# Performance work log

Measured on AMD Instinct MI355X. Metric: run time of the kernel, lower is better.

## Reference

```python
import jax, jax.numpy as jnp
import numpy as np
import math

NUM_CONVS = 4
GN_GROUPS = 32
GN_EPS = 1e-5
FPN_STRIDES = (8, 16, 32, 64, 128)
PRIOR_PROB = 0.01


def conv3x3(x, w, b):
    # x: [N,C,H,W], w: [O,I,3,3]
    y = jax.lax.conv_general_dilated(
        x, w, window_strides=(1, 1), padding='SAME',
        dimension_numbers=('NCHW', 'OIHW', 'NCHW'))
    return y + b[None, :, None, None]


def group_norm(x, gamma, beta):
    n, c, h, w = x.shape
    xg = x.reshape(n, GN_GROUPS, c // GN_GROUPS, h, w)
    mean = xg.mean(axis=(2, 3, 4), keepdims=True)
    var = xg.var(axis=(2, 3, 4), keepdims=True)
    xn = ((xg - mean) * jax.lax.rsqrt(var + GN_EPS)).reshape(n, c, h, w)
    return xn * gamma[None, :, None, None] + beta[None, :, None, None]


def subnet(x, ws, bs, gws, gbs):
    # NUM_CONVS x (conv3x3 -> GN -> ReLU)
    for i in range(NUM_CONVS):
        x = jax.nn.relu(group_norm(conv3x3(x, ws[i], bs[i]), gws[i], gbs[i]))
    return x


def permute_to_N_HWA_K(x, k):
    n = x.shape[0]
    return x.transpose(0, 2, 3, 1).reshape(n, -1, k)


def setup_inputs() -> dict:
    key = jax.random.key(0)
    ks = jax.random.split(key, 16)
    C, K = 256, 80
    feats = {
        'p3': jax.random.normal(ks[0], (1, C, 80, 80), jnp.float32),
        'p4': jax.random.normal(ks[1], (1, C, 40, 40), jnp.float32),
        'p5': jax.random.normal(ks[2], (1, C, 20, 20), jnp.float32),
        'p6': jax.random.normal(ks[3], (1, C, 10, 10), jnp.float32),
        'p7': jax.random.normal(ks[4], (1, C, 5, 5), jnp.float32),
    }
    std = 0.01
    bias_value = -math.log((1 - PRIOR_PROB) / PRIOR_PROB)
    params = {
        'cls_w': std * jax.random.normal(ks[5], (NUM_CONVS, C, C, 3, 3), jnp.float32),
        'cls_b': jnp.zeros((NUM_CONVS, C), jnp.float32),
        'cls_gn_w': jnp.ones((NUM_CONVS, C), jnp.float32),
        'cls_gn_b': jnp.zeros((NUM_CONVS, C), jnp.float32),
        'box_w': std * jax.random.normal(ks[6], (NUM_CONVS, C, C, 3, 3), jnp.float32),
        'box_b': jnp.zeros((NUM_CONVS, C), jnp.float32),
        'box_gn_w': jnp.ones((NUM_CONVS, C), jnp.float32),
        'box_gn_b': jnp.zeros((NUM_CONVS, C), jnp.float32),
        'score_w': std * jax.random.normal(ks[7], (K, C, 3, 3), jnp.float32),
        'score_b': jnp.full((K,), bias_value, jnp.float32),
        'pred_w': std * jax.random.normal(ks[8], (4, C, 3, 3), jnp.float32),
        'pred_b': jnp.zeros((4,), jnp.float32),
        'iou_w': std * jax.random.normal(ks[9], (1, C, 3, 3), jnp.float32),
        'iou_b': jnp.zeros((1,), jnp.float32),
        'scales': jnp.ones((5,), jnp.float32),
    }
    return {**feats, **params}


def reference(p3, p4, p5, p6, p7,
              cls_w, cls_b, cls_gn_w, cls_gn_b,
              box_w, box_b, box_gn_w, box_gn_b,
              score_w, score_b, pred_w, pred_b, iou_w, iou_b, scales):
    features = [p3, p4, p5, p6, p7]
    logits, bbox_reg, ious = [], [], []
    for l, feat in enumerate(features):
        c = subnet(feat, cls_w, cls_b, cls_gn_w, cls_gn_b)
        b = subnet(feat, box_w, box_b, box_gn_w, box_gn_b)
        logit = conv3x3(c, score_w, score_b)          # [N,80,H,W]
        iou = conv3x3(b, iou_w, iou_b)                # [N,1,H,W]
        bp = conv3x3(b, pred_w, pred_b) * scales[l]   # Scale module
        # norm_reg_targets=True branch
        reg = jax.nn.relu(bp) * FPN_STRIDES[l]        # [N,4,H,W]
        logits.append(permute_to_N_HWA_K(logit, 80))
        bbox_reg.append(permute_to_N_HWA_K(reg, 4))
        ious.append(permute_to_N_HWA_K(iou, 1))
    box_cls = jnp.concatenate(logits, axis=1)    # [N, sumHW, 80]
    box_delta = jnp.concatenate(bbox_reg, axis=1)  # [N, sumHW, 4]
    box_iou = jnp.concatenate(ious, axis=1)      # [N, sumHW, 1]
    # pack into one array for a single output: [N, sumHW, 85]
    return jnp.concatenate([box_cls, box_delta, box_iou], axis=-1)
```

## Files before the change

### kernel.cpp

```cpp
#include <hip/hip_runtime.h>

typedef unsigned short u16;
typedef __attribute__((ext_vector_type(8))) short bf16x8;
typedef __attribute__((ext_vector_type(4))) float f32x4;

#define NLEV 5
#define CCH 256
#define KTOT 2304
#define P_TOT 8525
#define PP_TOT 9165
#define PLS (PP_TOT*64)

__constant__ int   c_HW[NLEV]     = {6400, 1600, 400, 100, 25};
__constant__ int   c_W[NLEV]      = {80, 40, 20, 10, 5};
__constant__ int   c_off[NLEV]    = {0, 6400, 8000, 8400, 8500};
__constant__ int   c_poff[NLEV]   = {0, 6724, 8488, 8972, 9116};
__constant__ int   c_tls[NLEV+1]  = {0, 50, 65, 71, 73, 74};
__constant__ int   c_ntx[NLEV]    = {5, 3, 2, 1, 1};
__constant__ float c_stridef[NLEV]= {8.f, 16.f, 32.f, 64.f, 128.f};

__device__ __forceinline__ u16 f2bf(float f){
  union { float f; unsigned u; } v; v.f = f;
  unsigned r = v.u + 0x7fffu + ((v.u >> 16) & 1u);
  return (u16)(r >> 16);
}

__device__ __forceinline__ void g2l16(const u16* g, u16* l, int lane){
#if defined(__has_builtin)
#if __has_builtin(__builtin_amdgcn_global_load_lds)
  __builtin_amdgcn_global_load_lds(
      (const __attribute__((address_space(1))) unsigned int*)g,
      (__attribute__((address_space(3))) unsigned int*)l, 16, 0, 0);
  return;
#endif
#endif
  *(uint4*)(l + lane*8) = *(const uint4*)g;
}

#define WAIT_VM0_LGKM0 0x0070

template<int MODE>
__global__ __launch_bounds__(256, 2) void gemm_conv(
    const u16* __restrict__ Xc, const u16* __restrict__ Xb,
    const u16* __restrict__ Wc, const u16* __restrict__ Wb,
    const float* __restrict__ bc, const float* __restrict__ bb,
    float* __restrict__ Yc, float* __restrict__ Yb,
    float* __restrict__ stats,
    const float* __restrict__ predb, const float* __restrict__ ioub,
    const float* __restrict__ scales, float* __restrict__ out)
{
  __shared__ u16 sA0[8192], sA1[8192];
  __shared__ u16 hB0[23*512], hB1[23*512];
  __shared__ float sstat[16][2];

  const int ptile = blockIdx.x;
  const int mtile = (MODE == 0) ? blockIdx.y : 0;
  const int br = blockIdx.z;
  int lv = 0;
  #pragma unroll
  for (int i = 1; i < NLEV; i++) if (ptile >= c_tls[i]) lv = i;
  const int tidx = ptile - c_tls[lv];
  const int ntx = c_ntx[lv];
  const int ty0 = (tidx / ntx) * 8, tx0 = (tidx - (tidx / ntx) * ntx) * 16;
  const int W = c_W[lv], wrow2 = W + 2;

  const int tid = threadIdx.x, wv = tid >> 6, ln = tid & 63;
  const int quad = ln >> 4, l15 = ln & 15;
  const int m0w = (wv & 1) * 64;
  const int pyw = (wv >> 1) * 4;

  const u16* __restrict__ X  = br ? Xb : Xc;
  const u16* __restrict__ WA = br ? Wb : Wc;

  const int ASTRIDE = (MODE == 0) ? 16384 : 8192;
  const u16* abase = WA + (size_t)(((MODE == 0) ? mtile*16 : 0) + wv*4)*512 + ln*8;

  const u16* hptr[6]; int hnum = 0;
  #pragma unroll
  for (int i = 0; i < 6; i++) {
    const int j = wv + 4*i;
    if (j < 23) {
      const int item = j*64 + ln;
      int hp = item >> 3; if (hp >= 180) hp -= 180;
      const int g = item & 7;
      const int hy = hp / 18, hx = hp - hy*18;
      const int prow = c_poff[lv] + (ty0 + hy)*wrow2 + tx0 + hx;
      hptr[i] = X + (size_t)prow*64 + ((g ^ (hp & 7)) << 3);
      hnum = i + 1;
    }
  }

  auto stageA = [&](int cc, int tap, u16* dA) {
    const u16* as = abase + (size_t)(tap*4 + cc) * ASTRIDE;
    u16* da = dA + (wv*4)*512;
    #pragma unroll
    for (int j = 0; j < 4; j++) g2l16(as + j*512, da + j*512, ln);
  };
  auto stageH = [&](int cc, u16* dH) {
    const size_t cof = (size_t)cc * PLS;
    for (int i = 0; i < hnum; i++)
      g2l16(hptr[i] + cof, dH + (wv + 4*i)*512, ln);
  };

  f32x4 acc[4][4];
  #pragma unroll
  for (int i = 0; i < 4; i++)
    #pragma unroll
    for (int j = 0; j < 4; j++) acc[i][j] = (f32x4){0.f, 0.f, 0.f, 0.f};

  if (MODE == 0 && tid < 32) sstat[tid >> 1][tid & 1] = 0.f;

  auto kbody = [&](int t, const u16* rA, u16* wA2) {
    __builtin_amdgcn_sched_barrier(0);
    __builtin_amdgcn_s_waitcnt(WAIT_VM0_LGKM0);
    __builtin_amdgcn_sched_barrier(0);
    __builtin_amdgcn_s_barrier();
    __builtin_amdgcn_sched_barrier(0);
    const int cc = t / 9, tap = t - cc*9;
    if (t < 35) {
      const int t1 = t + 1, ncc = t1 / 9;
      stageA(ncc, t1 - ncc*9, wA2);
    }
    if (tap == 8 && cc < 3) stageH(cc + 1, ((cc + 1) & 1) ? hB1 : hB0);
    const u16* rB = (cc & 1) ? hB1 : hB0;
    const int dh = tap / 3, dw = tap - dh*3;
    bf16x8 af[2][4], bf[2][4];
    #pragma unroll
    for (int sub = 0; sub < 2; sub++) {
      const int swzA = ((sub*4 + quad) ^ (l15 & 7)) * 8;
      #pragma unroll
      for (int mt = 0; mt < 4; mt++)
        af[sub][mt] = *(const bf16x8*)&rA[(m0w + mt*16 + l15)*64 + swzA];
      #pragma unroll
      for (int nt = 0; nt < 4; nt++) {
        const int hp = (pyw + nt + dh)*18 + l15 + dw;
        const int gk = sub*4 + quad;
        bf[sub][nt] = *(const bf16x8*)&rB[hp*64 + ((gk ^ (hp & 7)) << 3)];
      }
    }
    #pragma unroll
    for (int sub = 0; sub < 2; sub++)
      #pragma unroll
      for (int mt = 0; mt < 4; mt++)
        #pragma unroll
        for (int nt = 0; nt < 4; nt++)
          acc[mt][nt] = __builtin_amdgcn_mfma_f32_16x16x32_bf16(
              af[sub][mt], bf[sub][nt], acc[mt][nt], 0, 0, 0);
  };

  stageH(0, hB0);
  stageA(0, 0, sA0);
  #pragma unroll 1
  for (int t = 0; t < 36; t += 2) {
    kbody(t,     sA0, sA1);
    kbody(t + 1, sA1, sA0);
  }

  const int gx = tx0 + l15;
  if (MODE == 0) {
    const float* __restrict__ bias = br ? bb : bc;
    float* __restrict__ Y = br ? Yb : Yc;
    #pragma unroll
    for (int mt = 0; mt < 4; mt++) {
      const int mloc = m0w + mt*16 + quad*4;
      const int mrow = mtile*128 + mloc;
      const f32x4 bv = *(const f32x4*)&bias[mrow];
      float s = 0.f, sq = 0.f;
      #pragma unroll
      for (int nt = 0; nt < 4; nt++) {
        const int gy = ty0 + pyw + nt;
        f32x4 v = acc[mt][nt] + bv;
        if (gy < W && gx < W) {
          const size_t n = (size_t)(c_off[lv] + gy*W + gx);
          *(f32x4*)&Y[n*CCH + mrow] = v;
          #pragma unroll
          for (int r = 0; r < 4; r++) { s += v[r]; sq += v[r]*v[r]; }
        }
      }
      #pragma unroll
      for (int o = 1; o < 16; o <<= 1) { s += __shfl_xor(s, o); sq += __shfl_xor(sq, o); }
      if (l15 == 0) {
        const int g = mloc >> 3;
        atomicAdd(&sstat[g][0], s);
        atomicAdd(&sstat[g][1], sq);
      }
    }
    __syncthreads();
    if (tid < 32) {
      const int g = tid >> 1, c = tid & 1;
      atomicAdd(&stats[((br*NLEV + lv)*32 + mtile*16 + g)*2 + c], sstat[g][c]);
    }
  } else {
    const float scl = scales[lv];
    const float stf = c_stridef[lv];
    #pragma unroll
    for (int mt = 0; mt < 4; mt++) {
      const int mr0 = m0w + mt*16 + quad*4;
      if (mr0 >= 85) continue;
      #pragma unroll
      for (int nt = 0; nt < 4; nt++) {
        const int gy = ty0 + pyw + nt;
        if (gy >= W || gx >= W) continue;
        const size_t n = (size_t)(c_off[lv] + gy*W + gx);
        const f32x4 v = acc[mt][nt];
        #pragma unroll
        for (int r = 0; r < 4; r++) {
          const int m = mr0 + r;
          if (br == 0) {
            if (m < 80) out[n*85 + m] = v[r] + bc[m];
          } else {
            if (m < 4) {
              const float t = (v[r] + predb[m]) * scl;
              out[n*85 + 80 + m] = fmaxf(t, 0.f) * stf;
            } else if (m == 4) {
              out[n*85 + 84] = v[r] + ioub[0];
            }
          }
        }
      }
    }
  }
}

__global__ __launch_bounds__(256) void gn_relu(
    const float* __restrict__ Yc, const float* __restrict__ Yb,
    const float* __restrict__ stats,
    const float* __restrict__ gwc, const float* __restrict__ gbc,
    const float* __restrict__ gwb, const float* __restrict__ gbb,
    u16* __restrict__ Xc, u16* __restrict__ Xb)
{
  const int t = blockIdx.x * 256 + threadIdx.x;
  if (t >= 2 * P_TOT * 32) return;
  const int br = t / (P_TOT * 32);
  const int r  = t - br * (P_TOT * 32);
  const int pg = r >> 5;
  const int c0 = (r & 31) << 3;
  int lv = 0;
  #pragma unroll
  for (int i = 1; i < NLEV; i++) if (pg >= c_off[i]) lv = i;
  const int pl = pg - c_off[lv];
  const int Wl = c_W[lv];
  const int g = c0 >> 3;
  const float* st = &stats[(((size_t)br*NLEV + lv)*32 + g)*2];
  const float cnt = 8.f * (float)c_HW[lv];
  const float mean = st[0] / cnt;
  const float var  = st[1] / cnt - mean*mean;
  const float rstd = rsqrtf(var + 1e-5f);
  const float* Y  = br ? Yb : Yc;
  const float* gw = br ? gwb : gwc;
  const float* gb = br ? gbb : gbc;
  u16* X = br ? Xb : Xc;
  const float* y = &Y[(size_t)pg*CCH + c0];
  const int h = pl / Wl, wi = pl - h*Wl;
  const size_t pidx = (size_t)(c_poff[lv] + (h+1)*(Wl+2) + (wi+1));
  union { u16 u[8]; uint4 v; } pk;
  #pragma unroll
  for (int i = 0; i < 8; i++) {
    const float v = (y[i] - mean)*rstd*gw[c0+i] + gb[c0+i];
    pk.u[i] = f2bf(fmaxf(v, 0.f));
  }
  *(uint4*)&X[(size_t)(c0 >> 6)*PLS + pidx*64 + (c0 & 63)] = pk.v;
}

__global__ __launch_bounds__(256) void feat2bf(
    const float* __restrict__ p3, const float* __restrict__ p4,
    const float* __restrict__ p5, const float* __restrict__ p6,
    const float* __restrict__ p7, u16* __restrict__ X)
{
  const int t = blockIdx.x * 256 + threadIdx.x;
  if (t >= P_TOT * 32) return;
  const int pg = t >> 5, c0 = (t & 31) << 3;
  int lv = 0;
  #pragma unroll
  for (int i = 1; i < NLEV; i++) if (pg >= c_off[i]) lv = i;
  const int pl = pg - c_off[lv];
  const float* src = lv==0 ? p3 : lv==1 ? p4 : lv==2 ? p5 : lv==3 ? p6 : p7;
  const int HW = c_HW[lv], Wl = c_W[lv];
  const int h = pl / Wl, wi = pl - h*Wl;
  const size_t pidx = (size_t)(c_poff[lv] + (h+1)*(Wl+2) + (wi+1));
  union { u16 u[8]; uint4 v; } pk;
  #pragma unroll
  for (int i = 0; i < 8; i++)
    pk.u[i] = f2bf(src[(size_t)(c0+i)*HW + pl]);
  *(uint4*)&X[(size_t)(c0 >> 6)*PLS + pidx*64 + (c0 & 63)] = pk.v;
}

__global__ __launch_bounds__(256) void wconv(
    const float* __restrict__ cw, const float* __restrict__ bw,
    u16* __restrict__ Wc, u16* __restrict__ Wb)
{
  const size_t N = (size_t)4*256*KTOT;
  const size_t t = (size_t)blockIdx.x * 256 + threadIdx.x;
  if (t >= 2*N) return;
  const float* src = (t < N) ? cw : bw;
  u16* dst = (t < N) ? Wc : Wb;
  const size_t i = (t < N) ? t : t - N;
  const size_t lc = i / KTOT;
  const int kk = (int)(i - lc*KTOT);
  const int l = (int)(lc >> 8), co = (int)(lc & 255);
  const int tap = kk >> 8, ci = kk & 255;
  const int s = kk >> 6, kl = kk & 63;
  const int r = co & 7, p = (kl >> 3) ^ r;
  const size_t d = (size_t)l*589824 +
      ((size_t)((s*32 + (co >> 3))*64 + r*8 + p))*8 + (kl & 7);
  dst[d] = f2bf(src[(lc*256 + ci)*9 + tap]);
}

__global__ __launch_bounds__(256) void hconv(
    const float* __restrict__ sw, const float* __restrict__ pw,
    const float* __restrict__ iw, u16* __restrict__ Whc, u16* __restrict__ Whb)
{
  const int N = 128 * KTOT;
  const int t = blockIdx.x * 256 + threadIdx.x;
  if (t >= 2*N) return;
  const int i = (t < N) ? t : t - N;
  const int co = i / KTOT, kk = i - co*KTOT;
  const int tap = kk >> 8, ci = kk & 255;
  const int s = kk >> 6, kl = kk & 63;
  const int r = co & 7, p = (kl >> 3) ^ r;
  const size_t d = ((size_t)((s*16 + (co >> 3))*64 + r*8 + p))*8 + (kl & 7);
  float v = 0.f;
  if (t < N) {
    if (co < 80) v = sw[(co*256 + ci)*9 + tap];
    Whc[d] = f2bf(v);
  } else {
    if (co < 4)       v = pw[(co*256 + ci)*9 + tap];
    else if (co == 4) v = iw[ci*9 + tap];
    Whb[d] = f2bf(v);
  }
}

extern "C" void kernel_launch(void* const* d_in, const int* in_sizes, int n_in,
                              void* d_out, int out_size, void* d_ws, size_t ws_size,
                              hipStream_t stream)
{
  const float* p3      = (const float*)d_in[0];
  const float* p4      = (const float*)d_in[1];
  const float* p5      = (const float*)d_in[2];
  const float* p6      = (const float*)d_in[3];
  const float* p7      = (const float*)d_in[4];
  const float* cls_w   = (const float*)d_in[5];
  const float* cls_b   = (const float*)d_in[6];
  const float* cls_gw  = (const float*)d_in[7];
  const float* cls_gb  = (const float*)d_in[8];
  const float* box_w   = (const float*)d_in[9];
  const float* box_b   = (const float*)d_in[10];
  const float* box_gw  = (const float*)d_in[11];
  const float* box_gb  = (const float*)d_in[12];
  const float* score_w = (const float*)d_in[13];
  const float* score_b = (const float*)d_in[14];
  const float* pred_w  = (const float*)d_in[15];
  const float* pred_b  = (const float*)d_in[16];
  const float* iou_w   = (const float*)d_in[17];
  const float* iou_b   = (const float*)d_in[18];
  const float* scales  = (const float*)d_in[19];
  float* out = (float*)d_out;

  char* w = (char*)d_ws;
  size_t o = 0;
  auto alloc = [&](size_t b) { void* p = w + o; o += (b + 255) & ~(size_t)255; return p; };
  u16*   XF = (u16*)alloc((size_t)PP_TOT*CCH*2);
  u16*   XC = (u16*)alloc((size_t)PP_TOT*CCH*2);
  u16*   XB = (u16*)alloc((size_t)PP_TOT*CCH*2);
  float* ST = (float*)alloc((size_t)4*2*NLEV*32*2*4);
  u16*  WRC = (u16*)alloc((size_t)4*256*KTOT*2);
  u16*  WRB = (u16*)alloc((size_t)4*256*KTOT*2);
  u16*  WHC = (u16*)alloc((size_t)128*KTOT*2);
  u16*  WHB = (u16*)alloc((size_t)128*KTOT*2);
  float* YC = (float*)alloc((size_t)P_TOT*CCH*4);
  float* YB = (float*)alloc((size_t)P_TOT*CCH*4);

  hipMemsetAsync(XF, 0, (size_t)3*PP_TOT*CCH*2 + (size_t)4*2*NLEV*32*2*4, stream);

  wconv<<<dim3((unsigned)(((size_t)2*4*256*KTOT + 255)/256)), 256, 0, stream>>>(cls_w, box_w, WRC, WRB);
  hconv<<<dim3((2*128*KTOT + 255)/256), 256, 0, stream>>>(score_w, pred_w, iou_w, WHC, WHB);
  feat2bf<<<dim3((P_TOT*32 + 255)/256), 256, 0, stream>>>(p3, p4, p5, p6, p7, XF);

  const u16* xci = XF; const u16* xbi = XF;
  for (int l = 0; l < 4; l++) {
    float* STl = ST + (size_t)l*2*NLEV*32*2;
    gemm_conv<0><<<dim3(74, 2, 2), 256, 0, stream>>>(
        xci, xbi, WRC + (size_t)l*589824, WRB + (size_t)l*589824,
        cls_b + l*256, box_b + l*256, YC, YB, STl,
        nullptr, nullptr, nullptr, nullptr);
    gn_relu<<<dim3((2*P_TOT*32 + 255)/256), 256, 0, stream>>>(
        YC, YB, STl, cls_gw + l*256, cls_gb + l*256, box_gw + l*256, box_gb + l*256,
        XC, XB);
    xci = XC; xbi = XB;
  }
  gemm_conv<1><<<dim3(74, 1, 2), 256, 0, stream>>>(
      xci, xbi, WHC, WHB, score_b, nullptr, nullptr, nullptr, nullptr,
      pred_b, iou_b, scales, out);
}
```

Measured before the change: 367.0 us.

## Cover all output channels per block, preload full input halo, barrier-free per-wave weight pipeline

Each conv block now covers all 256 output channels for its 8x16 pixel tile, which halves the grid and removes the duplicate halo loads across the two M-tiles. All four channel chunks of the input halo are loaded into LDS up front. Each wave double-buffers its own weight slice using vmcnt waits and no block-wide barriers. In exchange the kernel uses far more LDS and registers (launch bounds drop to one block per SIMD group). The grid also shrinks to 148 blocks, which risks underfilling the GPU's compute units.

```diff
diff --git a/kernel.cpp b/kernel.cpp
--- a/kernel.cpp
+++ b/kernel.cpp
@@ -10,6 +10,7 @@
 #define P_TOT 8525
 #define PP_TOT 9165
 #define PLS (PP_TOT*64)
+#define HSTR 11776
 
 __constant__ int   c_HW[NLEV]     = {6400, 1600, 400, 100, 25};
 __constant__ int   c_W[NLEV]      = {80, 40, 20, 10, 5};
@@ -37,10 +38,12 @@
   *(uint4*)(l + lane*8) = *(const uint4*)g;
 }
 
-#define WAIT_VM0_LGKM0 0x0070
+#define WAIT_VM8   0x0F78
+#define WAIT_VM0   0x0F70
+#define WAIT_LGKM0 0xC07F
 
 template<int MODE>
-__global__ __launch_bounds__(256, 2) void gemm_conv(
+__global__ __launch_bounds__(256, 1) void gemm_conv(
     const u16* __restrict__ Xc, const u16* __restrict__ Xb,
     const u16* __restrict__ Wc, const u16* __restrict__ Wb,
     const float* __restrict__ bc, const float* __restrict__ bb,
@@ -49,13 +52,12 @@
     const float* __restrict__ predb, const float* __restrict__ ioub,
     const float* __restrict__ scales, float* __restrict__ out)
 {
-  __shared__ u16 sA0[8192], sA1[8192];
-  __shared__ u16 hB0[23*512], hB1[23*512];
-  __shared__ float sstat[16][2];
-
-  const int ptile = blockIdx.x;
-  const int mtile = (MODE == 0) ? blockIdx.y : 0;
-  const int br = blockIdx.z;
+  constexpr int NT = (MODE == 0) ? 8 : 4;
+  __shared__ u16 hB[4*HSTR];
+  __shared__ u16 sA[4][2][4096];
+  __shared__ float sstat[32][2];
+
+  const int ptile = blockIdx.x, br = blockIdx.z;
   int lv = 0;
   #pragma unroll
   for (int i = 1; i < NLEV; i++) if (ptile >= c_tls[i]) lv = i;
@@ -66,14 +68,12 @@
 
   const int tid = threadIdx.x, wv = tid >> 6, ln = tid & 63;
   const int quad = ln >> 4, l15 = ln & 15;
-  const int m0w = (wv & 1) * 64;
-  const int pyw = (wv >> 1) * 4;
 
   const u16* __restrict__ X  = br ? Xb : Xc;
   const u16* __restrict__ WA = br ? Wb : Wc;
 
-  const int ASTRIDE = (MODE == 0) ? 16384 : 8192;
-  const u16* abase = WA + (size_t)(((MODE == 0) ? mtile*16 : 0) + wv*4)*512 + ln*8;
+  const int ASTR = (MODE == 0) ? 16384 : 8192;
+  const u16* abase = WA + (size_t)(((MODE == 0) ? wv : (wv & 1)) * 8) * 512 + ln*8;
 
   const u16* hptr[6]; int hnum = 0;
   #pragma unroll
@@ -90,70 +90,67 @@
     }
   }
 
-  auto stageA = [&](int cc, int tap, u16* dA) {
-    const u16* as = abase + (size_t)(tap*4 + cc) * ASTRIDE;
-    u16* da = dA + (wv*4)*512;
-    #pragma unroll
-    for (int j = 0; j < 4; j++) g2l16(as + j*512, da + j*512, ln);
+  auto stageA = [&](int s, int b) {
+    const u16* as = abase + (size_t)s * ASTR;
+    u16* da = &sA[wv][b][0];
+    #pragma unroll
+    for (int j = 0; j < 8; j++) g2l16(as + j*512, da + j*512, ln);
   };
-  auto stageH = [&](int cc, u16* dH) {
-    const size_t cof = (size_t)cc * PLS;
-    for (int i = 0; i < hnum; i++)
-      g2l16(hptr[i] + cof, dH + (wv + 4*i)*512, ln);
-  };
-
-  f32x4 acc[4][4];
+
+  f32x4 acc[4][NT];
   #pragma unroll
   for (int i = 0; i < 4; i++)
     #pragma unroll
-    for (int j = 0; j < 4; j++) acc[i][j] = (f32x4){0.f, 0.f, 0.f, 0.f};
-
-  if (MODE == 0 && tid < 32) sstat[tid >> 1][tid & 1] = 0.f;
-
-  auto kbody = [&](int t, const u16* rA, u16* wA2) {
-    __builtin_amdgcn_sched_barrier(0);
-    __builtin_amdgcn_s_waitcnt(WAIT_VM0_LGKM0);
-    __builtin_amdgcn_sched_barrier(0);
-    __builtin_amdgcn_s_barrier();
-    __builtin_amdgcn_sched_barrier(0);
+    for (int j = 0; j < NT; j++) acc[i][j] = (f32x4){0.f, 0.f, 0.f, 0.f};
+
+  if (MODE == 0 && tid < 64) sstat[tid >> 1][tid & 1] = 0.f;
+
+  for (int i = 0; i < hnum; i++) {
+    const int j = wv + 4*i;
+    #pragma unroll
+    for (int cc = 0; cc < 4; cc++)
+      g2l16(hptr[i] + (size_t)cc*PLS, hB + cc*HSTR + j*512, ln);
+  }
+  stageA(0, 0);
+  __syncthreads();
+  stageA(4, 1);
+
+  #pragma unroll 1
+  for (int t = 0; t < 36; t++) {
+    if (t < 35) __builtin_amdgcn_s_waitcnt(WAIT_VM8);
+    else        __builtin_amdgcn_s_waitcnt(WAIT_VM0);
     const int cc = t / 9, tap = t - cc*9;
-    if (t < 35) {
-      const int t1 = t + 1, ncc = t1 / 9;
-      stageA(ncc, t1 - ncc*9, wA2);
-    }
-    if (tap == 8 && cc < 3) stageH(cc + 1, ((cc + 1) & 1) ? hB1 : hB0);
-    const u16* rB = (cc & 1) ? hB1 : hB0;
     const int dh = tap / 3, dw = tap - dh*3;
-    bf16x8 af[2][4], bf[2][4];
+    const u16* myA = &sA[wv][t & 1][0];
+    const u16* hpl = &hB[cc * HSTR];
+    bf16x8 af[2][4], bf[2][NT];
     #pragma unroll
     for (int sub = 0; sub < 2; sub++) {
-      const int swzA = ((sub*4 + quad) ^ (l15 & 7)) * 8;
+      const int q = sub*4 + quad;
+      const int swzA = (q ^ (l15 & 7)) * 8;
       #pragma unroll
       for (int mt = 0; mt < 4; mt++)
-        af[sub][mt] = *(const bf16x8*)&rA[(m0w + mt*16 + l15)*64 + swzA];
-      #pragma unroll
-      for (int nt = 0; nt < 4; nt++) {
-        const int hp = (pyw + nt + dh)*18 + l15 + dw;
-        const int gk = sub*4 + quad;
-        bf[sub][nt] = *(const bf16x8*)&rB[hp*64 + ((gk ^ (hp & 7)) << 3)];
+        af[sub][mt] = *(const bf16x8*)&myA[(mt*16 + l15)*64 + swzA];
+      #pragma unroll
+      for (int nt = 0; nt < NT; nt++) {
+        const int py = (MODE == 0) ? nt : ((wv >> 1)*4 + nt);
+        const int hp = (py + dh)*18 + l15 + dw;
+        bf[sub][nt] = *(const bf16x8*)&hpl[hp*64 + ((q ^ (hp & 7)) << 3)];
       }
+    }
+    __builtin_amdgcn_s_waitcnt(WAIT_LGKM0);
+    if (t + 2 < 36) {
+      const int t2 = t + 2, cc2 = t2 / 9, tap2 = t2 - cc2*9;
+      stageA(tap2*4 + cc2, t & 1);
     }
     #pragma unroll
     for (int sub = 0; sub < 2; sub++)
       #pragma unroll
       for (int mt = 0; mt < 4; mt++)
         #pragma unroll
-        for (int nt = 0; nt < 4; nt++)
+        for (int nt = 0; nt < NT; nt++)
           acc[mt][nt] = __builtin_amdgcn_mfma_f32_16x16x32_bf16(
               af[sub][mt], bf[sub][nt], acc[mt][nt], 0, 0, 0);
-  };
-
-  stageH(0, hB0);
-  stageA(0, 0, sA0);
-  #pragma unroll 1
-  for (int t = 0; t < 36; t += 2) {
-    kbody(t,     sA0, sA1);
-    kbody(t + 1, sA1, sA0);
   }
 
   const int gx = tx0 + l15;
@@ -162,13 +159,12 @@
     float* __restrict__ Y = br ? Yb : Yc;
     #pragma unroll
     for (int mt = 0; mt < 4; mt++) {
-      const int mloc = m0w + mt*16 + quad*4;
-      const int mrow = mtile*128 + mloc;
+      const int mrow = wv*64 + mt*16 + quad*4;
       const f32x4 bv = *(const f32x4*)&bias[mrow];
       float s = 0.f, sq = 0.f;
       #pragma unroll
-      for (int nt = 0; nt < 4; nt++) {
-        const int gy = ty0 + pyw + nt;
+      for (int nt = 0; nt < NT; nt++) {
+        const int gy = ty0 + nt;
         f32x4 v = acc[mt][nt] + bv;
         if (gy < W && gx < W) {
           const size_t n = (size_t)(c_off[lv] + gy*W + gx);
@@ -180,26 +176,26 @@
       #pragma unroll
       for (int o = 1; o < 16; o <<= 1) { s += __shfl_xor(s, o); sq += __shfl_xor(sq, o); }
       if (l15 == 0) {
-        const int g = mloc >> 3;
+        const int g = mrow >> 3;
         atomicAdd(&sstat[g][0], s);
         atomicAdd(&sstat[g][1], sq);
       }
     }
     __syncthreads();
-    if (tid < 32) {
+    if (tid < 64) {
       const int g = tid >> 1, c = tid & 1;
-      atomicAdd(&stats[((br*NLEV + lv)*32 + mtile*16 + g)*2 + c], sstat[g][c]);
+      atomicAdd(&stats[((br*NLEV + lv)*32 + g)*2 + c], sstat[g][c]);
     }
   } else {
     const float scl = scales[lv];
     const float stf = c_stridef[lv];
     #pragma unroll
     for (int mt = 0; mt < 4; mt++) {
-      const int mr0 = m0w + mt*16 + quad*4;
+      const int mr0 = (wv & 1)*64 + mt*16 + quad*4;
       if (mr0 >= 85) continue;
       #pragma unroll
-      for (int nt = 0; nt < 4; nt++) {
-        const int gy = ty0 + pyw + nt;
+      for (int nt = 0; nt < NT; nt++) {
+        const int gy = ty0 + (wv >> 1)*4 + nt;
         if (gy >= W || gx >= W) continue;
         const size_t n = (size_t)(c_off[lv] + gy*W + gx);
         const f32x4 v = acc[mt][nt];
@@ -379,7 +375,7 @@
   const u16* xci = XF; const u16* xbi = XF;
   for (int l = 0; l < 4; l++) {
     float* STl = ST + (size_t)l*2*NLEV*32*2;
-    gemm_conv<0><<<dim3(74, 2, 2), 256, 0, stream>>>(
+    gemm_conv<0><<<dim3(74, 1, 2), 256, 0, stream>>>(
         xci, xbi, WRC + (size_t)l*589824, WRB + (size_t)l*589824,
         cls_b + l*256, box_b + l*256, YC, YB, STl,
         nullptr, nullptr, nullptr, nullptr);
```

New measurement: 374.0 us. Within noise of the previous version (+1.9%).
